# Performance work log

Measured on AMD Instinct MI355X. Metric: run time of the kernel, lower is better.

## Reference

```python
import jax, jax.numpy as jnp
import numpy as np

SINKHORN_ITERS = 10


def _optimal_transport(attn, phi, iters):
    # attn: [N,H,W,W], phi: scalar dustbin score
    bs, h, w, _ = attn.shape
    marginal = jnp.concatenate([jnp.ones((w,), attn.dtype), jnp.array([float(w)], attn.dtype)]) / (2.0 * w)
    log_mu = jnp.log(marginal)  # [W+1], broadcasts over [N,H,W+1]
    log_nu = log_mu
    # augment with dustbin row/col filled with phi -> [N,H,W+1,W+1]
    sim = jnp.concatenate([attn, jnp.broadcast_to(phi, (bs, h, w, 1))], axis=-1)
    sim = jnp.concatenate([sim, jnp.broadcast_to(phi, (bs, h, 1, w + 1))], axis=-2)

    def body(i, uv):
        u, v = uv
        v = log_nu - jax.nn.logsumexp(sim + u[..., :, None], axis=2)
        u = log_mu - jax.nn.logsumexp(sim + v[..., None, :], axis=3)
        return (u, v)

    u0 = jnp.zeros((bs, h, w + 1), attn.dtype)
    u, v = jax.lax.fori_loop(0, iters, body, (u0, u0))
    attn_ot = sim + u[..., :, None] + v[..., None, :]
    return jnp.exp(attn_ot + jnp.log(2.0 * w))


def _compute_low_res_disp(pos_shift, attn, occ_mask=None):
    # attn: [N,H,W,W] (dustbins removed); pos_shift: [W,W]
    w = attn.shape[-1]
    high_response = jnp.argmax(attn, axis=-1)  # [N,H,W]
    response_range = jnp.stack([high_response - 1, high_response, high_response + 1], axis=-1)  # [N,H,W,3]
    attn_pad = jnp.pad(attn, ((0, 0), (0, 0), (0, 0), (1, 1)))
    attn_rw = jnp.take_along_axis(attn_pad, response_range + 1, axis=-1)  # [N,H,W,3]
    norm = attn_rw.sum(-1, keepdims=True)
    norm = jnp.where(norm < 0.1, 1.0, norm)  # occ_mask is None branch
    attn_rw = attn_rw / norm
    pos_pad = jnp.pad(pos_shift, ((0, 0), (1, 1)))  # [W,W+2]
    pos_pad = jnp.broadcast_to(pos_pad[None, None], attn_pad.shape)
    pos_rw = jnp.take_along_axis(pos_pad, response_range + 1, axis=-1)
    disp = (attn_rw * pos_rw).sum(-1)  # [N,H,W]
    return disp, norm


def setup_inputs() -> dict:
    key = jax.random.key(0)
    k1, _ = jax.random.split(key)
    N, H, W = 4, 120, 256
    attn_weight = jax.random.normal(k1, (N, H, W, W), dtype=jnp.float32)
    phi = jnp.zeros((1,), dtype=jnp.float32)
    return {"attn_weight": attn_weight, "phi": phi}


def reference(attn_weight, phi):
    w = attn_weight.shape[2]
    attn_ot = _optimal_transport(attn_weight, phi[0], SINKHORN_ITERS)  # [N,H,W+1,W+1]
    # relative position shift, clamped at 0
    pos = jnp.arange(w, dtype=attn_weight.dtype)
    pos_shift = jnp.maximum(pos[:, None] - pos[None, :], 0.0)  # [W,W]
    disp_pred_low_res, matched_attn = _compute_low_res_disp(pos_shift, attn_ot[..., :-1, :-1], None)
    occ_pred = 1.0 - matched_attn.squeeze(-1)  # [N,H,W]
    return disp_pred_low_res, occ_pred
```

## Files before the change

kernel.cpp:

```cpp
#include <hip/hip_runtime.h>
#include <cstdint>

namespace {

constexpr int W = 256;
constexpr int ITERS = 10;
constexpr int PSTR = 260;
constexpr int NG = 16;

__global__ __launch_bounds__(1024)
void sinkhorn_disp_kernel(
    const float* __restrict__ attn,
    const float* __restrict__ phi_p,
    float* __restrict__ out,
    int nh)
{
  __shared__ __align__(16) float E_lds[1024 * 32];
  __shared__ __align__(16) float fpart[NG][PSTR];
  __shared__ __align__(16) float eu[W + 4];
  __shared__ __align__(16) float ev[W + 4];
  __shared__ __align__(16) float win[W][4];
  __shared__ int   jmax[W];
  __shared__ float Seu_s, Sev_s, ephi_s;

  const int tid = threadIdx.x;
  const int tc  = tid & 31;
  const int tr  = tid >> 5;
  const int bid = blockIdx.x;
  const int sw  = tid & 7;
  float* myE = &E_lds[tid * 32];
  #define RDCH(c) (*(const float4*)&myE[4 * ((c) ^ sw)])

  float Er[4][8];
  {
    const float* src = attn + (size_t)bid * (W * W) + (size_t)(tr * 8) * W + tc * 8;
    #pragma unroll
    for (int a = 0; a < 4; ++a) {
      float4 x0 = *(const float4*)(src + a * W);
      float4 x1 = *(const float4*)(src + a * W + 4);
      Er[a][0] = __expf(x0.x); Er[a][1] = __expf(x0.y);
      Er[a][2] = __expf(x0.z); Er[a][3] = __expf(x0.w);
      Er[a][4] = __expf(x1.x); Er[a][5] = __expf(x1.y);
      Er[a][6] = __expf(x1.z); Er[a][7] = __expf(x1.w);
    }
    #pragma unroll
    for (int ap = 0; ap < 4; ++ap) {
      float4 x0 = *(const float4*)(src + (4 + ap) * W);
      float4 x1 = *(const float4*)(src + (4 + ap) * W + 4);
      float4 e0 = make_float4(__expf(x0.x), __expf(x0.y), __expf(x0.z), __expf(x0.w));
      float4 e1 = make_float4(__expf(x1.x), __expf(x1.y), __expf(x1.z), __expf(x1.w));
      *(float4*)&myE[4 * ((2 * ap)     ^ sw)] = e0;
      *(float4*)&myE[4 * ((2 * ap + 1) ^ sw)] = e1;
    }
  }
  if (tid <= W) eu[tid] = 1.0f;
  if (tid == 0) ephi_s = __expf(phi_p[0]);
  __syncthreads();

  const float inv2w = 1.0f / (2.0f * W);

  for (int it = 0; it < ITERS; ++it) {
    {
      float4 u0 = *(const float4*)&eu[tr * 8];
      float4 u1 = *(const float4*)&eu[tr * 8 + 4];
      float ul[8] = {u0.x, u0.y, u0.z, u0.w, u1.x, u1.y, u1.z, u1.w};
      float cp[8];
      #pragma unroll
      for (int b = 0; b < 8; ++b) cp[b] = 0.0f;
      #pragma unroll
      for (int a = 0; a < 4; ++a) {
        #pragma unroll
        for (int b = 0; b < 8; ++b) cp[b] = __builtin_fmaf(Er[a][b], ul[a], cp[b]);
      }
      #pragma unroll
      for (int ap = 0; ap < 4; ++ap) {
        float4 e0 = RDCH(2 * ap), e1 = RDCH(2 * ap + 1);
        float ua = ul[4 + ap];
        cp[0] = __builtin_fmaf(e0.x, ua, cp[0]);
        cp[1] = __builtin_fmaf(e0.y, ua, cp[1]);
        cp[2] = __builtin_fmaf(e0.z, ua, cp[2]);
        cp[3] = __builtin_fmaf(e0.w, ua, cp[3]);
        cp[4] = __builtin_fmaf(e1.x, ua, cp[4]);
        cp[5] = __builtin_fmaf(e1.y, ua, cp[5]);
        cp[6] = __builtin_fmaf(e1.z, ua, cp[6]);
        cp[7] = __builtin_fmaf(e1.w, ua, cp[7]);
      }
      #pragma unroll
      for (int b = 0; b < 8; ++b) cp[b] += __shfl_xor(cp[b], 32, 64);
      if (!(tr & 1)) {
        float4* dst = (float4*)&fpart[tr >> 1][tc * 8];
        dst[0] = make_float4(cp[0], cp[1], cp[2], cp[3]);
        dst[1] = make_float4(cp[4], cp[5], cp[6], cp[7]);
      }
    }
    if (tid < 64) {
      float s = eu[tid] + eu[tid + 64] + eu[tid + 128] + eu[tid + 192];
      if (tid == 0) s += eu[W];
      #pragma unroll
      for (int off = 32; off > 0; off >>= 1) s += __shfl_xor(s, off, 64);
      if (tid == 0) Seu_s = s;
    }
    __syncthreads();
    if (tid < W) {
      float s = 0.0f;
      #pragma unroll
      for (int g = 0; g < NG; ++g) s += fpart[g][tid];
      s += ephi_s * eu[W];
      ev[tid] = inv2w / s;
    } else if (tid == W) {
      ev[W] = 0.5f / (ephi_s * Seu_s);
    }
    __syncthreads();
    {
      float4 v0 = *(const float4*)&ev[tc * 8];
      float4 v1 = *(const float4*)&ev[tc * 8 + 4];
      float vl[8] = {v0.x, v0.y, v0.z, v0.w, v1.x, v1.y, v1.z, v1.w};
      float rp[8];
      #pragma unroll
      for (int a = 0; a < 8; ++a) rp[a] = 0.0f;
      #pragma unroll
      for (int a = 0; a < 4; ++a) {
        #pragma unroll
        for (int b = 0; b < 8; ++b) rp[a] = __builtin_fmaf(Er[a][b], vl[b], rp[a]);
      }
      #pragma unroll
      for (int ap = 0; ap < 4; ++ap) {
        float4 e0 = RDCH(2 * ap), e1 = RDCH(2 * ap + 1);
        float s = e0.x * vl[0] + e0.y * vl[1] + e0.z * vl[2] + e0.w * vl[3]
                + e1.x * vl[4] + e1.y * vl[5] + e1.z * vl[6] + e1.w * vl[7];
        rp[4 + ap] = s;
      }
      #pragma unroll
      for (int a = 0; a < 8; ++a) rp[a] += __shfl_xor(rp[a], 16, 64);
      if (!(tc & 16)) {
        float4* dst = (float4*)&fpart[tc][tr * 8];
        dst[0] = make_float4(rp[0], rp[1], rp[2], rp[3]);
        dst[1] = make_float4(rp[4], rp[5], rp[6], rp[7]);
      }
    }
    if (tid < 64) {
      float s = ev[tid] + ev[tid + 64] + ev[tid + 128] + ev[tid + 192];
      if (tid == 0) s += ev[W];
      #pragma unroll
      for (int off = 32; off > 0; off >>= 1) s += __shfl_xor(s, off, 64);
      if (tid == 0) Sev_s = s;
    }
    __syncthreads();
    if (tid < W) {
      float s = 0.0f;
      #pragma unroll
      for (int g = 0; g < NG; ++g) s += fpart[g][tid];
      s += ephi_s * ev[W];
      eu[tid] = inv2w / s;
    } else if (tid == W) {
      eu[W] = 0.5f / (ephi_s * Sev_s);
    }
    __syncthreads();
  }

  if (tid < W) { win[tid][0] = 0.0f; win[tid][1] = 0.0f; win[tid][2] = 0.0f; }
  float vl[8];
  {
    float4 v0 = *(const float4*)&ev[tc * 8];
    float4 v1 = *(const float4*)&ev[tc * 8 + 4];
    vl[0] = v0.x; vl[1] = v0.y; vl[2] = v0.z; vl[3] = v0.w;
    vl[4] = v1.x; vl[5] = v1.y; vl[6] = v1.z; vl[7] = v1.w;
  }
  {
    #pragma unroll
    for (int a = 0; a < 8; ++a) {
      float m = -1.0f; int mj = 0;
      if (a < 4) {
        #pragma unroll
        for (int b = 0; b < 8; ++b) {
          float vv = Er[a < 4 ? a : 0][b] * vl[b];
          if (vv > m) { m = vv; mj = tc * 8 + b; }
        }
      } else {
        float4 e0 = RDCH(2 * (a - 4)), e1 = RDCH(2 * (a - 4) + 1);
        float e8[8] = {e0.x, e0.y, e0.z, e0.w, e1.x, e1.y, e1.z, e1.w};
        #pragma unroll
        for (int b = 0; b < 8; ++b) {
          float vv = e8[b] * vl[b];
          if (vv > m) { m = vv; mj = tc * 8 + b; }
        }
      }
      unsigned long long best =
          (((unsigned long long)__float_as_uint(m)) << 32) |
          (unsigned)(65535 - mj);
      #pragma unroll
      for (int off = 16; off > 0; off >>= 1) {
        unsigned long long o = __shfl_xor(best, off, 64);
        best = (o > best) ? o : best;
      }
      if (tc == 0) jmax[tr * 8 + a] = 65535 - (int)(best & 0xffffffffull);
    }
  }
  __syncthreads();
  {
    float4 u0 = *(const float4*)&eu[tr * 8];
    float4 u1 = *(const float4*)&eu[tr * 8 + 4];
    float ul[8] = {u0.x, u0.y, u0.z, u0.w, u1.x, u1.y, u1.z, u1.w};
    #pragma unroll
    for (int a = 0; a < 8; ++a) {
      int i  = tr * 8 + a;
      int jm = jmax[i];
      float e8[8];
      if (a < 4) {
        #pragma unroll
        for (int b = 0; b < 8; ++b) e8[b] = Er[a < 4 ? a : 0][b];
      } else {
        float4 e0 = RDCH(2 * (a - 4)), e1 = RDCH(2 * (a - 4) + 1);
        e8[0] = e0.x; e8[1] = e0.y; e8[2] = e0.z; e8[3] = e0.w;
        e8[4] = e1.x; e8[5] = e1.y; e8[6] = e1.z; e8[7] = e1.w;
      }
      #pragma unroll
      for (int b = 0; b < 8; ++b) {
        int k = (tc * 8 + b) - (jm - 1);
        if (k >= 0 && k < 3) {
          win[i][k] = e8[b] * vl[b] * ul[a] * (2.0f * W);
        }
      }
    }
  }
  __syncthreads();
  if (tid < W) {
    const int i  = tid;
    const int jm = jmax[i];
    float w0 = win[i][0], w1 = win[i][1], w2 = win[i][2];
    float norm0 = w0 + w1 + w2;
    float norm  = (norm0 < 0.1f) ? 1.0f : norm0;
    float p0 = fmaxf((float)(i - (jm - 1)), 0.0f);
    float p1 = fmaxf((float)(i - jm),       0.0f);
    float p2 = fmaxf((float)(i - (jm + 1)), 0.0f);
    float disp = (w0 / norm) * p0 + (w1 / norm) * p1 + (w2 / norm) * p2;
    float occ  = 1.0f - norm;
    out[(size_t)bid * W + i] = disp;
    out[(size_t)nh * W + (size_t)bid * W + i] = occ;
  }
  #undef RDCH
}

}

extern "C" void kernel_launch(void* const* d_in, const int* in_sizes, int n_in,
                              void* d_out, int out_size, void* d_ws, size_t ws_size,
                              hipStream_t stream) {
  (void)n_in; (void)d_ws; (void)ws_size; (void)out_size;
  const float* attn = (const float*)d_in[0];
  const float* phi  = (const float*)d_in[1];
  float* out = (float*)d_out;
  const int nh = in_sizes[0] / (W * W);
  sinkhorn_disp_kernel<<<dim3(nh), dim3(1024), 0, stream>>>(attn, phi, out, nh);
}
```

Measured before the change: 247.5 us.

## Halve block to 512 threads with 16 rows per thread, 12 kept in registers

Each block now uses 512 threads instead of 1024. Each thread owns 16 rows by 8 columns of the exp'd matrix: 12 rows live in registers and 4 rows in LDS. The column and row reduction trees change to match (NG=8, extra xor-8 shuffle), and the LDS used for the matrix copy is halved. The goal is to keep more of the matrix in registers, cut LDS traffic and partial-sum work, and possibly fit more blocks per CU. The cost is much higher register pressure (96 floats of Er per thread) and fewer threads to hide latency.

```diff
diff --git a/kernel.cpp b/kernel.cpp
--- a/kernel.cpp
+++ b/kernel.cpp
@@ -6,20 +6,20 @@
 constexpr int W = 256;
 constexpr int ITERS = 10;
 constexpr int PSTR = 260;
-constexpr int NG = 16;
-
-__global__ __launch_bounds__(1024)
+constexpr int NG = 8;
+
+__global__ __launch_bounds__(512, 4)
 void sinkhorn_disp_kernel(
     const float* __restrict__ attn,
     const float* __restrict__ phi_p,
     float* __restrict__ out,
     int nh)
 {
-  __shared__ __align__(16) float E_lds[1024 * 32];
+  __shared__ __align__(16) float E_lds[512 * 32];
   __shared__ __align__(16) float fpart[NG][PSTR];
   __shared__ __align__(16) float eu[W + 4];
   __shared__ __align__(16) float ev[W + 4];
-  __shared__ __align__(16) float win[W][4];
+  __shared__ float win[W][3];
   __shared__ int   jmax[W];
   __shared__ float Seu_s, Sev_s, ephi_s;
 
@@ -31,22 +31,22 @@
   float* myE = &E_lds[tid * 32];
   #define RDCH(c) (*(const float4*)&myE[4 * ((c) ^ sw)])
 
-  float Er[4][8];
+  float Er[12][8];
   {
-    const float* src = attn + (size_t)bid * (W * W) + (size_t)(tr * 8) * W + tc * 8;
-    #pragma unroll
-    for (int a = 0; a < 4; ++a) {
-      float4 x0 = *(const float4*)(src + a * W);
-      float4 x1 = *(const float4*)(src + a * W + 4);
-      Er[a][0] = __expf(x0.x); Er[a][1] = __expf(x0.y);
-      Er[a][2] = __expf(x0.z); Er[a][3] = __expf(x0.w);
-      Er[a][4] = __expf(x1.x); Er[a][5] = __expf(x1.y);
-      Er[a][6] = __expf(x1.z); Er[a][7] = __expf(x1.w);
+    const float* src = attn + (size_t)bid * (W * W) + (size_t)(tr * 16) * W + tc * 8;
+    #pragma unroll
+    for (int r = 0; r < 12; ++r) {
+      float4 x0 = *(const float4*)(src + r * W);
+      float4 x1 = *(const float4*)(src + r * W + 4);
+      Er[r][0] = __expf(x0.x); Er[r][1] = __expf(x0.y);
+      Er[r][2] = __expf(x0.z); Er[r][3] = __expf(x0.w);
+      Er[r][4] = __expf(x1.x); Er[r][5] = __expf(x1.y);
+      Er[r][6] = __expf(x1.z); Er[r][7] = __expf(x1.w);
     }
     #pragma unroll
     for (int ap = 0; ap < 4; ++ap) {
-      float4 x0 = *(const float4*)(src + (4 + ap) * W);
-      float4 x1 = *(const float4*)(src + (4 + ap) * W + 4);
+      float4 x0 = *(const float4*)(src + (12 + ap) * W);
+      float4 x1 = *(const float4*)(src + (12 + ap) * W + 4);
       float4 e0 = make_float4(__expf(x0.x), __expf(x0.y), __expf(x0.z), __expf(x0.w));
       float4 e1 = make_float4(__expf(x1.x), __expf(x1.y), __expf(x1.z), __expf(x1.w));
       *(float4*)&myE[4 * ((2 * ap)     ^ sw)] = e0;
@@ -61,29 +61,36 @@
 
   for (int it = 0; it < ITERS; ++it) {
     {
-      float4 u0 = *(const float4*)&eu[tr * 8];
-      float4 u1 = *(const float4*)&eu[tr * 8 + 4];
-      float ul[8] = {u0.x, u0.y, u0.z, u0.w, u1.x, u1.y, u1.z, u1.w};
       float cp[8];
       #pragma unroll
       for (int b = 0; b < 8; ++b) cp[b] = 0.0f;
       #pragma unroll
-      for (int a = 0; a < 4; ++a) {
-        #pragma unroll
-        for (int b = 0; b < 8; ++b) cp[b] = __builtin_fmaf(Er[a][b], ul[a], cp[b]);
-      }
-      #pragma unroll
-      for (int ap = 0; ap < 4; ++ap) {
-        float4 e0 = RDCH(2 * ap), e1 = RDCH(2 * ap + 1);
-        float ua = ul[4 + ap];
-        cp[0] = __builtin_fmaf(e0.x, ua, cp[0]);
-        cp[1] = __builtin_fmaf(e0.y, ua, cp[1]);
-        cp[2] = __builtin_fmaf(e0.z, ua, cp[2]);
-        cp[3] = __builtin_fmaf(e0.w, ua, cp[3]);
-        cp[4] = __builtin_fmaf(e1.x, ua, cp[4]);
-        cp[5] = __builtin_fmaf(e1.y, ua, cp[5]);
-        cp[6] = __builtin_fmaf(e1.z, ua, cp[6]);
-        cp[7] = __builtin_fmaf(e1.w, ua, cp[7]);
+      for (int q = 0; q < 3; ++q) {
+        float4 u = *(const float4*)&eu[tr * 16 + q * 4];
+        float uu[4] = {u.x, u.y, u.z, u.w};
+        #pragma unroll
+        for (int k = 0; k < 4; ++k) {
+          #pragma unroll
+          for (int b = 0; b < 8; ++b)
+            cp[b] = __builtin_fmaf(Er[q * 4 + k][b], uu[k], cp[b]);
+        }
+      }
+      {
+        float4 u = *(const float4*)&eu[tr * 16 + 12];
+        float uu[4] = {u.x, u.y, u.z, u.w};
+        #pragma unroll
+        for (int ap = 0; ap < 4; ++ap) {
+          float4 e0 = RDCH(2 * ap), e1 = RDCH(2 * ap + 1);
+          float ua = uu[ap];
+          cp[0] = __builtin_fmaf(e0.x, ua, cp[0]);
+          cp[1] = __builtin_fmaf(e0.y, ua, cp[1]);
+          cp[2] = __builtin_fmaf(e0.z, ua, cp[2]);
+          cp[3] = __builtin_fmaf(e0.w, ua, cp[3]);
+          cp[4] = __builtin_fmaf(e1.x, ua, cp[4]);
+          cp[5] = __builtin_fmaf(e1.y, ua, cp[5]);
+          cp[6] = __builtin_fmaf(e1.z, ua, cp[6]);
+          cp[7] = __builtin_fmaf(e1.w, ua, cp[7]);
+        }
       }
       #pragma unroll
       for (int b = 0; b < 8; ++b) cp[b] += __shfl_xor(cp[b], 32, 64);
@@ -115,27 +122,42 @@
       float4 v0 = *(const float4*)&ev[tc * 8];
       float4 v1 = *(const float4*)&ev[tc * 8 + 4];
       float vl[8] = {v0.x, v0.y, v0.z, v0.w, v1.x, v1.y, v1.z, v1.w};
-      float rp[8];
-      #pragma unroll
-      for (int a = 0; a < 8; ++a) rp[a] = 0.0f;
-      #pragma unroll
-      for (int a = 0; a < 4; ++a) {
-        #pragma unroll
-        for (int b = 0; b < 8; ++b) rp[a] = __builtin_fmaf(Er[a][b], vl[b], rp[a]);
-      }
-      #pragma unroll
-      for (int ap = 0; ap < 4; ++ap) {
-        float4 e0 = RDCH(2 * ap), e1 = RDCH(2 * ap + 1);
-        float s = e0.x * vl[0] + e0.y * vl[1] + e0.z * vl[2] + e0.w * vl[3]
-                + e1.x * vl[4] + e1.y * vl[5] + e1.z * vl[6] + e1.w * vl[7];
-        rp[4 + ap] = s;
-      }
-      #pragma unroll
-      for (int a = 0; a < 8; ++a) rp[a] += __shfl_xor(rp[a], 16, 64);
-      if (!(tc & 16)) {
-        float4* dst = (float4*)&fpart[tc][tr * 8];
-        dst[0] = make_float4(rp[0], rp[1], rp[2], rp[3]);
-        dst[1] = make_float4(rp[4], rp[5], rp[6], rp[7]);
+      #pragma unroll
+      for (int q = 0; q < 3; ++q) {
+        float rp[4];
+        #pragma unroll
+        for (int k = 0; k < 4; ++k) {
+          float s = 0.0f;
+          #pragma unroll
+          for (int b = 0; b < 8; ++b)
+            s = __builtin_fmaf(Er[q * 4 + k][b], vl[b], s);
+          rp[k] = s;
+        }
+        #pragma unroll
+        for (int k = 0; k < 4; ++k) {
+          rp[k] += __shfl_xor(rp[k], 16, 64);
+          rp[k] += __shfl_xor(rp[k], 8, 64);
+        }
+        if (tc < 8)
+          *(float4*)&fpart[tc][tr * 16 + q * 4] =
+              make_float4(rp[0], rp[1], rp[2], rp[3]);
+      }
+      {
+        float rp[4];
+        #pragma unroll
+        for (int ap = 0; ap < 4; ++ap) {
+          float4 e0 = RDCH(2 * ap), e1 = RDCH(2 * ap + 1);
+          rp[ap] = e0.x * vl[0] + e0.y * vl[1] + e0.z * vl[2] + e0.w * vl[3]
+                 + e1.x * vl[4] + e1.y * vl[5] + e1.z * vl[6] + e1.w * vl[7];
+        }
+        #pragma unroll
+        for (int k = 0; k < 4; ++k) {
+          rp[k] += __shfl_xor(rp[k], 16, 64);
+          rp[k] += __shfl_xor(rp[k], 8, 64);
+        }
+        if (tc < 8)
+          *(float4*)&fpart[tc][tr * 16 + 12] =
+              make_float4(rp[0], rp[1], rp[2], rp[3]);
       }
     }
     if (tid < 64) {
@@ -166,59 +188,59 @@
     vl[0] = v0.x; vl[1] = v0.y; vl[2] = v0.z; vl[3] = v0.w;
     vl[4] = v1.x; vl[5] = v1.y; vl[6] = v1.z; vl[7] = v1.w;
   }
-  {
-    #pragma unroll
-    for (int a = 0; a < 8; ++a) {
-      float m = -1.0f; int mj = 0;
-      if (a < 4) {
-        #pragma unroll
-        for (int b = 0; b < 8; ++b) {
-          float vv = Er[a < 4 ? a : 0][b] * vl[b];
-          if (vv > m) { m = vv; mj = tc * 8 + b; }
-        }
-      } else {
-        float4 e0 = RDCH(2 * (a - 4)), e1 = RDCH(2 * (a - 4) + 1);
-        float e8[8] = {e0.x, e0.y, e0.z, e0.w, e1.x, e1.y, e1.z, e1.w};
-        #pragma unroll
-        for (int b = 0; b < 8; ++b) {
-          float vv = e8[b] * vl[b];
-          if (vv > m) { m = vv; mj = tc * 8 + b; }
-        }
-      }
-      unsigned long long best =
-          (((unsigned long long)__float_as_uint(m)) << 32) |
-          (unsigned)(65535 - mj);
-      #pragma unroll
-      for (int off = 16; off > 0; off >>= 1) {
-        unsigned long long o = __shfl_xor(best, off, 64);
-        best = (o > best) ? o : best;
-      }
-      if (tc == 0) jmax[tr * 8 + a] = 65535 - (int)(best & 0xffffffffull);
-    }
+  #pragma unroll
+  for (int r = 0; r < 16; ++r) {
+    float e8[8];
+    if (r < 12) {
+      #pragma unroll
+      for (int b = 0; b < 8; ++b) e8[b] = Er[r < 12 ? r : 0][b];
+    } else {
+      float4 e0 = RDCH(2 * (r - 12)), e1 = RDCH(2 * (r - 12) + 1);
+      e8[0] = e0.x; e8[1] = e0.y; e8[2] = e0.z; e8[3] = e0.w;
+      e8[4] = e1.x; e8[5] = e1.y; e8[6] = e1.z; e8[7] = e1.w;
+    }
+    float m = -1.0f; int mj = 0;
+    #pragma unroll
+    for (int b = 0; b < 8; ++b) {
+      float vv = e8[b] * vl[b];
+      if (vv > m) { m = vv; mj = tc * 8 + b; }
+    }
+    unsigned long long best =
+        (((unsigned long long)__float_as_uint(m)) << 32) |
+        (unsigned)(65535 - mj);
+    #pragma unroll
+    for (int off = 16; off > 0; off >>= 1) {
+      unsigned long long o = __shfl_xor(best, off, 64);
+      best = (o > best) ? o : best;
+    }
+    if (tc == 0) jmax[tr * 16 + r] = 65535 - (int)(best & 0xffffffffull);
   }
   __syncthreads();
   {
-    float4 u0 = *(const float4*)&eu[tr * 8];
-    float4 u1 = *(const float4*)&eu[tr * 8 + 4];
-    float ul[8] = {u0.x, u0.y, u0.z, u0.w, u1.x, u1.y, u1.z, u1.w};
-    #pragma unroll
-    for (int a = 0; a < 8; ++a) {
-      int i  = tr * 8 + a;
-      int jm = jmax[i];
-      float e8[8];
-      if (a < 4) {
-        #pragma unroll
-        for (int b = 0; b < 8; ++b) e8[b] = Er[a < 4 ? a : 0][b];
-      } else {
-        float4 e0 = RDCH(2 * (a - 4)), e1 = RDCH(2 * (a - 4) + 1);
-        e8[0] = e0.x; e8[1] = e0.y; e8[2] = e0.z; e8[3] = e0.w;
-        e8[4] = e1.x; e8[5] = e1.y; e8[6] = e1.z; e8[7] = e1.w;
-      }
-      #pragma unroll
-      for (int b = 0; b < 8; ++b) {
-        int k = (tc * 8 + b) - (jm - 1);
-        if (k >= 0 && k < 3) {
-          win[i][k] = e8[b] * vl[b] * ul[a] * (2.0f * W);
+    #pragma unroll
+    for (int q = 0; q < 4; ++q) {
+      float4 u = *(const float4*)&eu[tr * 16 + q * 4];
+      float uu[4] = {u.x, u.y, u.z, u.w};
+      #pragma unroll
+      for (int k = 0; k < 4; ++k) {
+        const int r = q * 4 + k;
+        const int i = tr * 16 + r;
+        const int jm = jmax[i];
+        float e8[8];
+        if (r < 12) {
+          #pragma unroll
+          for (int b = 0; b < 8; ++b) e8[b] = Er[r < 12 ? r : 0][b];
+        } else {
+          float4 e0 = RDCH(2 * (r - 12)), e1 = RDCH(2 * (r - 12) + 1);
+          e8[0] = e0.x; e8[1] = e0.y; e8[2] = e0.z; e8[3] = e0.w;
+          e8[4] = e1.x; e8[5] = e1.y; e8[6] = e1.z; e8[7] = e1.w;
+        }
+        #pragma unroll
+        for (int b = 0; b < 8; ++b) {
+          int kk = (tc * 8 + b) - (jm - 1);
+          if (kk >= 0 && kk < 3) {
+            win[i][kk] = e8[b] * vl[b] * uu[k] * (2.0f * W);
+          }
         }
       }
     }
@@ -251,5 +273,5 @@
   const float* phi  = (const float*)d_in[1];
   float* out = (float*)d_out;
   const int nh = in_sizes[0] / (W * W);
-  sinkhorn_disp_kernel<<<dim3(nh), dim3(1024), 0, stream>>>(attn, phi, out, nh);
+  sinkhorn_disp_kernel<<<dim3(nh), dim3(512), 0, stream>>>(attn, phi, out, nh);
 }
```

Result: slower. 437.9 us (+77.0%).

## Keep the full 8x8 exp tile in registers instead of spilling half to LDS

Applied to the files above, without the earlier changes.

Each thread now holds all 64 exponentiated attention values in VGPRs rather than keeping four rows in registers and four in a 128 KB LDS buffer. This removes the LDS reads in every Sinkhorn matvec and in the argmax/window passes, and frees most of the shared memory. The launch bound now requests more waves per EU, which caps VGPR usage and may force spills of the 64-element tile. The padded window array is also shrunk.

```diff
diff --git a/kernel.cpp b/kernel.cpp
--- a/kernel.cpp
+++ b/kernel.cpp
@@ -8,18 +8,17 @@
 constexpr int PSTR = 260;
 constexpr int NG = 16;
 
-__global__ __launch_bounds__(1024)
+__global__ __launch_bounds__(1024, 4)
 void sinkhorn_disp_kernel(
     const float* __restrict__ attn,
     const float* __restrict__ phi_p,
     float* __restrict__ out,
     int nh)
 {
-  __shared__ __align__(16) float E_lds[1024 * 32];
   __shared__ __align__(16) float fpart[NG][PSTR];
   __shared__ __align__(16) float eu[W + 4];
   __shared__ __align__(16) float ev[W + 4];
-  __shared__ __align__(16) float win[W][4];
+  __shared__ float win[W][3];
   __shared__ int   jmax[W];
   __shared__ float Seu_s, Sev_s, ephi_s;
 
@@ -27,15 +26,12 @@
   const int tc  = tid & 31;
   const int tr  = tid >> 5;
   const int bid = blockIdx.x;
-  const int sw  = tid & 7;
-  float* myE = &E_lds[tid * 32];
-  #define RDCH(c) (*(const float4*)&myE[4 * ((c) ^ sw)])
-
-  float Er[4][8];
+
+  float Er[8][8];
   {
     const float* src = attn + (size_t)bid * (W * W) + (size_t)(tr * 8) * W + tc * 8;
     #pragma unroll
-    for (int a = 0; a < 4; ++a) {
+    for (int a = 0; a < 8; ++a) {
       float4 x0 = *(const float4*)(src + a * W);
       float4 x1 = *(const float4*)(src + a * W + 4);
       Er[a][0] = __expf(x0.x); Er[a][1] = __expf(x0.y);
@@ -43,15 +39,6 @@
       Er[a][4] = __expf(x1.x); Er[a][5] = __expf(x1.y);
       Er[a][6] = __expf(x1.z); Er[a][7] = __expf(x1.w);
     }
-    #pragma unroll
-    for (int ap = 0; ap < 4; ++ap) {
-      float4 x0 = *(const float4*)(src + (4 + ap) * W);
-      float4 x1 = *(const float4*)(src + (4 + ap) * W + 4);
-      float4 e0 = make_float4(__expf(x0.x), __expf(x0.y), __expf(x0.z), __expf(x0.w));
-      float4 e1 = make_float4(__expf(x1.x), __expf(x1.y), __expf(x1.z), __expf(x1.w));
-      *(float4*)&myE[4 * ((2 * ap)     ^ sw)] = e0;
-      *(float4*)&myE[4 * ((2 * ap + 1) ^ sw)] = e1;
-    }
   }
   if (tid <= W) eu[tid] = 1.0f;
   if (tid == 0) ephi_s = __expf(phi_p[0]);
@@ -68,22 +55,10 @@
       #pragma unroll
       for (int b = 0; b < 8; ++b) cp[b] = 0.0f;
       #pragma unroll
-      for (int a = 0; a < 4; ++a) {
+      for (int a = 0; a < 8; ++a) {
         #pragma unroll
-        for (int b = 0; b < 8; ++b) cp[b] = __builtin_fmaf(Er[a][b], ul[a], cp[b]);
-      }
-      #pragma unroll
-      for (int ap = 0; ap < 4; ++ap) {
-        float4 e0 = RDCH(2 * ap), e1 = RDCH(2 * ap + 1);
-        float ua = ul[4 + ap];
-        cp[0] = __builtin_fmaf(e0.x, ua, cp[0]);
-        cp[1] = __builtin_fmaf(e0.y, ua, cp[1]);
-        cp[2] = __builtin_fmaf(e0.z, ua, cp[2]);
-        cp[3] = __builtin_fmaf(e0.w, ua, cp[3]);
-        cp[4] = __builtin_fmaf(e1.x, ua, cp[4]);
-        cp[5] = __builtin_fmaf(e1.y, ua, cp[5]);
-        cp[6] = __builtin_fmaf(e1.z, ua, cp[6]);
-        cp[7] = __builtin_fmaf(e1.w, ua, cp[7]);
+        for (int b = 0; b < 8; ++b)
+          cp[b] = __builtin_fmaf(Er[a][b], ul[a], cp[b]);
       }
       #pragma unroll
       for (int b = 0; b < 8; ++b) cp[b] += __shfl_xor(cp[b], 32, 64);
@@ -117,18 +92,12 @@
       float vl[8] = {v0.x, v0.y, v0.z, v0.w, v1.x, v1.y, v1.z, v1.w};
       float rp[8];
       #pragma unroll
-      for (int a = 0; a < 8; ++a) rp[a] = 0.0f;
-      #pragma unroll
-      for (int a = 0; a < 4; ++a) {
+      for (int a = 0; a < 8; ++a) {
+        float s = 0.0f;
         #pragma unroll
-        for (int b = 0; b < 8; ++b) rp[a] = __builtin_fmaf(Er[a][b], vl[b], rp[a]);
-      }
-      #pragma unroll
-      for (int ap = 0; ap < 4; ++ap) {
-        float4 e0 = RDCH(2 * ap), e1 = RDCH(2 * ap + 1);
-        float s = e0.x * vl[0] + e0.y * vl[1] + e0.z * vl[2] + e0.w * vl[3]
-                + e1.x * vl[4] + e1.y * vl[5] + e1.z * vl[6] + e1.w * vl[7];
-        rp[4 + ap] = s;
+        for (int b = 0; b < 8; ++b)
+          s = __builtin_fmaf(Er[a][b], vl[b], s);
+        rp[a] = s;
       }
       #pragma unroll
       for (int a = 0; a < 8; ++a) rp[a] += __shfl_xor(rp[a], 16, 64);
@@ -166,35 +135,23 @@
     vl[0] = v0.x; vl[1] = v0.y; vl[2] = v0.z; vl[3] = v0.w;
     vl[4] = v1.x; vl[5] = v1.y; vl[6] = v1.z; vl[7] = v1.w;
   }
-  {
-    #pragma unroll
-    for (int a = 0; a < 8; ++a) {
-      float m = -1.0f; int mj = 0;
-      if (a < 4) {
-        #pragma unroll
-        for (int b = 0; b < 8; ++b) {
-          float vv = Er[a < 4 ? a : 0][b] * vl[b];
-          if (vv > m) { m = vv; mj = tc * 8 + b; }
-        }
-      } else {
-        float4 e0 = RDCH(2 * (a - 4)), e1 = RDCH(2 * (a - 4) + 1);
-        float e8[8] = {e0.x, e0.y, e0.z, e0.w, e1.x, e1.y, e1.z, e1.w};
-        #pragma unroll
-        for (int b = 0; b < 8; ++b) {
-          float vv = e8[b] * vl[b];
-          if (vv > m) { m = vv; mj = tc * 8 + b; }
-        }
-      }
-      unsigned long long best =
-          (((unsigned long long)__float_as_uint(m)) << 32) |
-          (unsigned)(65535 - mj);
-      #pragma unroll
-      for (int off = 16; off > 0; off >>= 1) {
-        unsigned long long o = __shfl_xor(best, off, 64);
-        best = (o > best) ? o : best;
-      }
-      if (tc == 0) jmax[tr * 8 + a] = 65535 - (int)(best & 0xffffffffull);
-    }
+  #pragma unroll
+  for (int a = 0; a < 8; ++a) {
+    float m = -1.0f; int mj = 0;
+    #pragma unroll
+    for (int b = 0; b < 8; ++b) {
+      float vv = Er[a][b] * vl[b];
+      if (vv > m) { m = vv; mj = tc * 8 + b; }
+    }
+    unsigned long long best =
+        (((unsigned long long)__float_as_uint(m)) << 32) |
+        (unsigned)(65535 - mj);
+    #pragma unroll
+    for (int off = 16; off > 0; off >>= 1) {
+      unsigned long long o = __shfl_xor(best, off, 64);
+      best = (o > best) ? o : best;
+    }
+    if (tc == 0) jmax[tr * 8 + a] = 65535 - (int)(best & 0xffffffffull);
   }
   __syncthreads();
   {
@@ -203,22 +160,13 @@
     float ul[8] = {u0.x, u0.y, u0.z, u0.w, u1.x, u1.y, u1.z, u1.w};
     #pragma unroll
     for (int a = 0; a < 8; ++a) {
-      int i  = tr * 8 + a;
-      int jm = jmax[i];
-      float e8[8];
-      if (a < 4) {
-        #pragma unroll
-        for (int b = 0; b < 8; ++b) e8[b] = Er[a < 4 ? a : 0][b];
-      } else {
-        float4 e0 = RDCH(2 * (a - 4)), e1 = RDCH(2 * (a - 4) + 1);
-        e8[0] = e0.x; e8[1] = e0.y; e8[2] = e0.z; e8[3] = e0.w;
-        e8[4] = e1.x; e8[5] = e1.y; e8[6] = e1.z; e8[7] = e1.w;
-      }
+      const int i  = tr * 8 + a;
+      const int jm = jmax[i];
       #pragma unroll
       for (int b = 0; b < 8; ++b) {
         int k = (tc * 8 + b) - (jm - 1);
         if (k >= 0 && k < 3) {
-          win[i][k] = e8[b] * vl[b] * ul[a] * (2.0f * W);
+          win[i][k] = Er[a][b] * vl[b] * ul[a] * (2.0f * W);
         }
       }
     }
@@ -238,7 +186,6 @@
     out[(size_t)bid * W + i] = disp;
     out[(size_t)nh * W + (size_t)bid * W + i] = occ;
   }
-  #undef RDCH
 }
 
 }
```

Measured after the change: 369.5 us. +49.3%, slower.

## Keep row scalings in registers and replace LDS reductions with DPP/swizzle

Applied to the files above, without the earlier changes.

The row-scaling vector u now lives in registers. The row-sum phase reduces within 32-lane halves using DPP and ds_swizzle all-reduces instead of staging partials in LDS, which removes two barriers per Sinkhorn iteration. The column-sum partials use a swizzled fpart layout and a two-thread-per-column split, divides become v_rcp approximations, and the final argmax/window/disp epilogue is done with in-wave reductions with no LDS or barriers. The risks are lower reciprocal precision and more cross-lane shuffle instructions per iteration.

```diff
diff --git a/kernel.cpp b/kernel.cpp
--- a/kernel.cpp
+++ b/kernel.cpp
@@ -6,7 +6,32 @@
 constexpr int W = 256;
 constexpr int ITERS = 10;
 constexpr int PSTR = 260;
-constexpr int NG = 16;
+
+__device__ __forceinline__ float dpp_add_xor1(float x) {
+  int y = __builtin_amdgcn_mov_dpp(__float_as_int(x), 0xB1, 0xF, 0xF, true);
+  return x + __int_as_float(y);
+}
+__device__ __forceinline__ float dpp_add_xor2(float x) {
+  int y = __builtin_amdgcn_mov_dpp(__float_as_int(x), 0x4E, 0xF, 0xF, true);
+  return x + __int_as_float(y);
+}
+template <int PAT>
+__device__ __forceinline__ float swz_add(float x) {
+  return x + __int_as_float(__builtin_amdgcn_ds_swizzle(__float_as_int(x), PAT));
+}
+__device__ __forceinline__ float allred32(float x) {
+  x = dpp_add_xor1(x);
+  x = dpp_add_xor2(x);
+  x = swz_add<0x101F>(x);
+  x = swz_add<0x201F>(x);
+  x = swz_add<0x401F>(x);
+  return x;
+}
+__device__ __forceinline__ float rcpf(float x) {
+  float r;
+  asm("v_rcp_f32 %0, %1" : "=v"(r) : "v"(x));
+  return r;
+}
 
 __global__ __launch_bounds__(1024)
 void sinkhorn_disp_kernel(
@@ -16,12 +41,10 @@
     int nh)
 {
   __shared__ __align__(16) float E_lds[1024 * 32];
-  __shared__ __align__(16) float fpart[NG][PSTR];
-  __shared__ __align__(16) float eu[W + 4];
-  __shared__ __align__(16) float ev[W + 4];
-  __shared__ __align__(16) float win[W][4];
-  __shared__ int   jmax[W];
-  __shared__ float Seu_s, Sev_s, ephi_s;
+  __shared__ __align__(16) float fpart[16][PSTR];
+  __shared__ __align__(16) float ev_l[W];
+  __shared__ __align__(16) float seup[32];
+  __shared__ float evW_s;
 
   const int tid = threadIdx.x;
   const int tc  = tid & 31;
@@ -31,6 +54,11 @@
   float* myE = &E_lds[tid * 32];
   #define RDCH(c) (*(const float4*)&myE[4 * ((c) ^ sw)])
 
+  const float ephi  = __expf(phi_p[0]);
+  const float inv2w = 1.0f / (2.0f * W);
+
+  const int ch0 = 4 * ((2 * tc) ^ ((tc >> 2) & 7));
+
   float Er[4][8];
   {
     const float* src = attn + (size_t)bid * (W * W) + (size_t)(tr * 8) * W + tc * 8;
@@ -47,35 +75,33 @@
     for (int ap = 0; ap < 4; ++ap) {
       float4 x0 = *(const float4*)(src + (4 + ap) * W);
       float4 x1 = *(const float4*)(src + (4 + ap) * W + 4);
-      float4 e0 = make_float4(__expf(x0.x), __expf(x0.y), __expf(x0.z), __expf(x0.w));
-      float4 e1 = make_float4(__expf(x1.x), __expf(x1.y), __expf(x1.z), __expf(x1.w));
-      *(float4*)&myE[4 * ((2 * ap)     ^ sw)] = e0;
-      *(float4*)&myE[4 * ((2 * ap + 1) ^ sw)] = e1;
-    }
-  }
-  if (tid <= W) eu[tid] = 1.0f;
-  if (tid == 0) ephi_s = __expf(phi_p[0]);
-  __syncthreads();
-
-  const float inv2w = 1.0f / (2.0f * W);
+      *(float4*)&myE[4 * ((2 * ap)     ^ sw)] =
+          make_float4(__expf(x0.x), __expf(x0.y), __expf(x0.z), __expf(x0.w));
+      *(float4*)&myE[4 * ((2 * ap + 1) ^ sw)] =
+          make_float4(__expf(x1.x), __expf(x1.y), __expf(x1.z), __expf(x1.w));
+    }
+  }
+
+  float eul[8];
+  #pragma unroll
+  for (int a = 0; a < 8; ++a) eul[a] = 1.0f;
+  float euW = 1.0f;
 
   for (int it = 0; it < ITERS; ++it) {
     {
-      float4 u0 = *(const float4*)&eu[tr * 8];
-      float4 u1 = *(const float4*)&eu[tr * 8 + 4];
-      float ul[8] = {u0.x, u0.y, u0.z, u0.w, u1.x, u1.y, u1.z, u1.w};
       float cp[8];
       #pragma unroll
       for (int b = 0; b < 8; ++b) cp[b] = 0.0f;
       #pragma unroll
       for (int a = 0; a < 4; ++a) {
         #pragma unroll
-        for (int b = 0; b < 8; ++b) cp[b] = __builtin_fmaf(Er[a][b], ul[a], cp[b]);
+        for (int b = 0; b < 8; ++b)
+          cp[b] = __builtin_fmaf(Er[a][b], eul[a], cp[b]);
       }
       #pragma unroll
       for (int ap = 0; ap < 4; ++ap) {
         float4 e0 = RDCH(2 * ap), e1 = RDCH(2 * ap + 1);
-        float ua = ul[4 + ap];
+        float ua = eul[4 + ap];
         cp[0] = __builtin_fmaf(e0.x, ua, cp[0]);
         cp[1] = __builtin_fmaf(e0.y, ua, cp[1]);
         cp[2] = __builtin_fmaf(e0.z, ua, cp[2]);
@@ -88,155 +114,119 @@
       #pragma unroll
       for (int b = 0; b < 8; ++b) cp[b] += __shfl_xor(cp[b], 32, 64);
       if (!(tr & 1)) {
-        float4* dst = (float4*)&fpart[tr >> 1][tc * 8];
-        dst[0] = make_float4(cp[0], cp[1], cp[2], cp[3]);
-        dst[1] = make_float4(cp[4], cp[5], cp[6], cp[7]);
-      }
-    }
-    if (tid < 64) {
-      float s = eu[tid] + eu[tid + 64] + eu[tid + 128] + eu[tid + 192];
-      if (tid == 0) s += eu[W];
-      #pragma unroll
-      for (int off = 32; off > 0; off >>= 1) s += __shfl_xor(s, off, 64);
-      if (tid == 0) Seu_s = s;
+        *(float4*)&fpart[tr >> 1][ch0    ] = make_float4(cp[0], cp[1], cp[2], cp[3]);
+        *(float4*)&fpart[tr >> 1][ch0 ^ 4] = make_float4(cp[4], cp[5], cp[6], cp[7]);
+      }
+      if (tc == 0)
+        seup[tr] = ((eul[0] + eul[1]) + (eul[2] + eul[3]))
+                 + ((eul[4] + eul[5]) + (eul[6] + eul[7]));
     }
     __syncthreads();
-    if (tid < W) {
+    if (tid < 2 * W) {
+      const int j  = tid >> 1;
+      const int fj = ((((j >> 2) ^ ((j >> 5) & 7)) << 2) | (j & 3));
+      const int g0 = (tid & 1) * 8;
       float s = 0.0f;
       #pragma unroll
-      for (int g = 0; g < NG; ++g) s += fpart[g][tid];
-      s += ephi_s * eu[W];
-      ev[tid] = inv2w / s;
-    } else if (tid == W) {
-      ev[W] = 0.5f / (ephi_s * Seu_s);
+      for (int g = 0; g < 8; ++g) s += fpart[g0 + g][fj];
+      s = dpp_add_xor1(s);
+      if (!(tid & 1)) ev_l[fj] = inv2w * rcpf(s + ephi * euW);
+    } else if ((tid >> 6) == 8) {
+      float s = allred32(seup[tid & 31]);
+      if (tid == 512) evW_s = 0.5f * rcpf(ephi * (s + euW));
     }
     __syncthreads();
     {
-      float4 v0 = *(const float4*)&ev[tc * 8];
-      float4 v1 = *(const float4*)&ev[tc * 8 + 4];
+      const float evW = evW_s;
+      float4 v0 = *(const float4*)&ev_l[ch0];
+      float4 v1 = *(const float4*)&ev_l[ch0 ^ 4];
       float vl[8] = {v0.x, v0.y, v0.z, v0.w, v1.x, v1.y, v1.z, v1.w};
       float rp[8];
       #pragma unroll
-      for (int a = 0; a < 8; ++a) rp[a] = 0.0f;
-      #pragma unroll
       for (int a = 0; a < 4; ++a) {
+        float s = 0.0f;
         #pragma unroll
-        for (int b = 0; b < 8; ++b) rp[a] = __builtin_fmaf(Er[a][b], vl[b], rp[a]);
+        for (int b = 0; b < 8; ++b)
+          s = __builtin_fmaf(Er[a][b], vl[b], s);
+        rp[a] = s;
       }
       #pragma unroll
       for (int ap = 0; ap < 4; ++ap) {
         float4 e0 = RDCH(2 * ap), e1 = RDCH(2 * ap + 1);
-        float s = e0.x * vl[0] + e0.y * vl[1] + e0.z * vl[2] + e0.w * vl[3]
-                + e1.x * vl[4] + e1.y * vl[5] + e1.z * vl[6] + e1.w * vl[7];
-        rp[4 + ap] = s;
-      }
-      #pragma unroll
-      for (int a = 0; a < 8; ++a) rp[a] += __shfl_xor(rp[a], 16, 64);
-      if (!(tc & 16)) {
-        float4* dst = (float4*)&fpart[tc][tr * 8];
-        dst[0] = make_float4(rp[0], rp[1], rp[2], rp[3]);
-        dst[1] = make_float4(rp[4], rp[5], rp[6], rp[7]);
-      }
-    }
-    if (tid < 64) {
-      float s = ev[tid] + ev[tid + 64] + ev[tid + 128] + ev[tid + 192];
-      if (tid == 0) s += ev[W];
-      #pragma unroll
-      for (int off = 32; off > 0; off >>= 1) s += __shfl_xor(s, off, 64);
-      if (tid == 0) Sev_s = s;
-    }
-    __syncthreads();
-    if (tid < W) {
-      float s = 0.0f;
-      #pragma unroll
-      for (int g = 0; g < NG; ++g) s += fpart[g][tid];
-      s += ephi_s * ev[W];
-      eu[tid] = inv2w / s;
-    } else if (tid == W) {
-      eu[W] = 0.5f / (ephi_s * Sev_s);
-    }
-    __syncthreads();
-  }
-
-  if (tid < W) { win[tid][0] = 0.0f; win[tid][1] = 0.0f; win[tid][2] = 0.0f; }
+        rp[4 + ap] = e0.x * vl[0] + e0.y * vl[1] + e0.z * vl[2] + e0.w * vl[3]
+                   + e1.x * vl[4] + e1.y * vl[5] + e1.z * vl[6] + e1.w * vl[7];
+      }
+      float sev = ((vl[0] + vl[1]) + (vl[2] + vl[3]))
+                + ((vl[4] + vl[5]) + (vl[6] + vl[7]));
+      #pragma unroll
+      for (int a = 0; a < 8; ++a) rp[a] = allred32(rp[a]);
+      sev = allred32(sev);
+      const float eAdd = ephi * evW;
+      #pragma unroll
+      for (int a = 0; a < 8; ++a) eul[a] = inv2w * rcpf(rp[a] + eAdd);
+      euW = 0.5f * rcpf(ephi * (sev + evW));
+    }
+  }
+
   float vl[8];
   {
-    float4 v0 = *(const float4*)&ev[tc * 8];
-    float4 v1 = *(const float4*)&ev[tc * 8 + 4];
+    float4 v0 = *(const float4*)&ev_l[ch0];
+    float4 v1 = *(const float4*)&ev_l[ch0 ^ 4];
     vl[0] = v0.x; vl[1] = v0.y; vl[2] = v0.z; vl[3] = v0.w;
     vl[4] = v1.x; vl[5] = v1.y; vl[6] = v1.z; vl[7] = v1.w;
   }
-  {
-    #pragma unroll
-    for (int a = 0; a < 8; ++a) {
-      float m = -1.0f; int mj = 0;
-      if (a < 4) {
-        #pragma unroll
-        for (int b = 0; b < 8; ++b) {
-          float vv = Er[a < 4 ? a : 0][b] * vl[b];
-          if (vv > m) { m = vv; mj = tc * 8 + b; }
-        }
-      } else {
-        float4 e0 = RDCH(2 * (a - 4)), e1 = RDCH(2 * (a - 4) + 1);
-        float e8[8] = {e0.x, e0.y, e0.z, e0.w, e1.x, e1.y, e1.z, e1.w};
-        #pragma unroll
-        for (int b = 0; b < 8; ++b) {
-          float vv = e8[b] * vl[b];
-          if (vv > m) { m = vv; mj = tc * 8 + b; }
-        }
-      }
-      unsigned long long best =
-          (((unsigned long long)__float_as_uint(m)) << 32) |
-          (unsigned)(65535 - mj);
-      #pragma unroll
-      for (int off = 16; off > 0; off >>= 1) {
-        unsigned long long o = __shfl_xor(best, off, 64);
-        best = (o > best) ? o : best;
-      }
-      if (tc == 0) jmax[tr * 8 + a] = 65535 - (int)(best & 0xffffffffull);
-    }
-  }
-  __syncthreads();
-  {
-    float4 u0 = *(const float4*)&eu[tr * 8];
-    float4 u1 = *(const float4*)&eu[tr * 8 + 4];
-    float ul[8] = {u0.x, u0.y, u0.z, u0.w, u1.x, u1.y, u1.z, u1.w};
-    #pragma unroll
-    for (int a = 0; a < 8; ++a) {
-      int i  = tr * 8 + a;
-      int jm = jmax[i];
-      float e8[8];
-      if (a < 4) {
-        #pragma unroll
-        for (int b = 0; b < 8; ++b) e8[b] = Er[a < 4 ? a : 0][b];
-      } else {
-        float4 e0 = RDCH(2 * (a - 4)), e1 = RDCH(2 * (a - 4) + 1);
-        e8[0] = e0.x; e8[1] = e0.y; e8[2] = e0.z; e8[3] = e0.w;
-        e8[4] = e1.x; e8[5] = e1.y; e8[6] = e1.z; e8[7] = e1.w;
-      }
-      #pragma unroll
-      for (int b = 0; b < 8; ++b) {
-        int k = (tc * 8 + b) - (jm - 1);
-        if (k >= 0 && k < 3) {
-          win[i][k] = e8[b] * vl[b] * ul[a] * (2.0f * W);
-        }
-      }
-    }
-  }
-  __syncthreads();
-  if (tid < W) {
-    const int i  = tid;
-    const int jm = jmax[i];
-    float w0 = win[i][0], w1 = win[i][1], w2 = win[i][2];
-    float norm0 = w0 + w1 + w2;
-    float norm  = (norm0 < 0.1f) ? 1.0f : norm0;
-    float p0 = fmaxf((float)(i - (jm - 1)), 0.0f);
-    float p1 = fmaxf((float)(i - jm),       0.0f);
-    float p2 = fmaxf((float)(i - (jm + 1)), 0.0f);
-    float disp = (w0 / norm) * p0 + (w1 / norm) * p1 + (w2 / norm) * p2;
-    float occ  = 1.0f - norm;
-    out[(size_t)bid * W + i] = disp;
-    out[(size_t)nh * W + (size_t)bid * W + i] = occ;
+  float res_disp = 0.0f, res_occ = 0.0f;
+  #pragma unroll
+  for (int a = 0; a < 8; ++a) {
+    float v[8];
+    if (a < 4) {
+      #pragma unroll
+      for (int b = 0; b < 8; ++b) v[b] = Er[a < 4 ? a : 0][b] * vl[b];
+    } else {
+      float4 e0 = RDCH(2 * (a - 4)), e1 = RDCH(2 * (a - 4) + 1);
+      v[0] = e0.x * vl[0]; v[1] = e0.y * vl[1];
+      v[2] = e0.z * vl[2]; v[3] = e0.w * vl[3];
+      v[4] = e1.x * vl[4]; v[5] = e1.y * vl[5];
+      v[6] = e1.z * vl[6]; v[7] = e1.w * vl[7];
+    }
+    float m = v[0]; int mj = tc * 8;
+    #pragma unroll
+    for (int b = 1; b < 8; ++b) {
+      if (v[b] > m) { m = v[b]; mj = tc * 8 + b; }
+    }
+    unsigned long long best =
+        (((unsigned long long)__float_as_uint(m)) << 32) |
+        (unsigned)(65535 - mj);
+    #pragma unroll
+    for (int off = 16; off > 0; off >>= 1) {
+      unsigned long long o = __shfl_xor(best, off, 32);
+      if (o > best) best = o;
+    }
+    const int jm = 65535 - (int)(best & 0xffffffffull);
+    const int i  = tr * 8 + a;
+    const float us = eul[a] * (2.0f * W);
+    float num = 0.0f, den = 0.0f;
+    #pragma unroll
+    for (int b = 0; b < 8; ++b) {
+      int j = tc * 8 + b;
+      if (j >= jm - 1 && j <= jm + 1) {
+        float w = v[b] * us;
+        den += w;
+        num += w * fmaxf((float)(i - j), 0.0f);
+      }
+    }
+    den = allred32(den);
+    num = allred32(num);
+    if (tc == a) {
+      float norm = (den < 0.1f) ? 1.0f : den;
+      res_disp = num / norm;
+      res_occ  = 1.0f - norm;
+    }
+  }
+  if (tc < 8) {
+    const int i = tr * 8 + tc;
+    out[(size_t)bid * W + i] = res_disp;
+    out[(size_t)nh * W + (size_t)bid * W + i] = res_occ;
   }
   #undef RDCH
 }
```

Result: faster. 241.1 us (-2.6%).
